# Kernel tuning notes

Measured on AMD Instinct MI355X. Metric: run time of the kernel, lower is better.

Reference implementation:

```python
import jax, jax.numpy as jnp
import numpy as np

N, D, H, L = 50000, 64, 4, 3
HD = D // H
E = 800000
EPS = 1e-5


def _layernorm(x, g, b):
    m = x.mean(-1, keepdims=True)
    v = ((x - m) ** 2).mean(-1, keepdims=True)
    return (x - m) * jax.lax.rsqrt(v + EPS) * g + b


def setup_inputs() -> dict:
    key = jax.random.key(0)
    ks = jax.random.split(key, 24)
    s = 0.05
    inp = {
        'feats': jax.random.normal(ks[0], (N, D), jnp.float32),
        'edge_index': jax.random.randint(ks[1], (2, E), 0, N, jnp.int64),
        'edge_attr': jax.random.uniform(ks[2], (E,), jnp.float32),
    }
    names = ['Wq', 'Wk', 'Wv', 'Wo', 'W1', 'W2']
    for i, n in enumerate(names):
        inp[n] = jax.random.normal(ks[3 + i], (L, D, D), jnp.float32) * s
    bnames = ['bq', 'bk', 'bv', 'bo', 'b1', 'b2']
    for i, n in enumerate(bnames):
        inp[n] = jnp.zeros((L, D), jnp.float32)
    inp['g1'] = jnp.ones((L, D), jnp.float32)
    inp['be1'] = jnp.zeros((L, D), jnp.float32)
    inp['g2'] = jnp.ones((L, D), jnp.float32)
    inp['be2'] = jnp.zeros((L, D), jnp.float32)
    return inp


def reference(feats, edge_index, edge_attr, Wq, bq, Wk, bk, Wv, bv, Wo, bo,
              W1, b1, W2, b2, g1, be1, g2, be2):
    row, col = edge_index[0], edge_index[1]  # source, destination nodes
    inv_sqrt = 1.0 / np.sqrt(HD).astype(np.float32)
    outs = []
    for l in range(L):
        # multi-head edge-indexed dot-product attention
        q = (feats @ Wq[l] + bq[l]).reshape(N, H, HD)
        k = (feats @ Wk[l] + bk[l]).reshape(N, H, HD)
        v = (feats @ Wv[l] + bv[l]).reshape(N, H, HD)
        scores = (q[col] * k[row]).sum(-1) * inv_sqrt       # [E, H]
        scores = scores * edge_attr[:, None]                # mult_attr modulation
        smax = jax.ops.segment_max(scores, col, num_segments=N)
        alpha = jnp.exp(scores - smax[col])
        denom = jax.ops.segment_sum(alpha, col, num_segments=N)
        alpha = alpha / denom[col]                          # scatter softmax
        agg = jax.ops.segment_sum(alpha[:, :, None] * v[row], col, num_segments=N)
        att = agg.reshape(N, D) @ Wo[l] + bo[l]
        feats = _layernorm(feats + att, g1[l], be1[l])      # res1 + norm1
        mlp = jax.nn.relu(feats @ W1[l] + b1[l]) @ W2[l] + b2[l]
        feats = _layernorm(feats + mlp, g2[l], be2[l])      # res2 + norm2
        outs.append(feats)
    return jnp.stack(outs)  # [L, N, D]
```

## Files before the change

kernel.cpp:

```cpp
#include <hip/hip_runtime.h>

#define NN 50000
#define DIM 64
#define NHEAD 4
#define NEDGE 800000
#define NLAYER 3
#define LN_EPS 1e-5f
#define SCAN_BLOCKS ((NN + 255) / 256)
#define ROWS 8

__device__ __forceinline__ float bcast(float x, int l) {
    return __uint_as_float(__builtin_amdgcn_readlane(__float_as_uint(x), l));
}

__device__ __forceinline__ unsigned int bf16rtn(float x) {
    unsigned int u = __float_as_uint(x);
    return (u + 0x7FFFu + ((u >> 16) & 1u)) >> 16;
}
__device__ __forceinline__ float blo(unsigned int u) {
    return __uint_as_float(u << 16);
}
__device__ __forceinline__ float bhi(unsigned int u) {
    return __uint_as_float(u & 0xFFFF0000u);
}


__global__ __launch_bounds__(256) void zero_kernel(int* __restrict__ p, int n) {
    int i = blockIdx.x * blockDim.x + threadIdx.x;
    if (i < n) p[i] = 0;
}

__global__ __launch_bounds__(256) void deg_kernel(const int* __restrict__ ei,
                                                  int* __restrict__ deg) {
    int e = blockIdx.x * blockDim.x + threadIdx.x;
    if (e < NEDGE) atomicAdd(&deg[ei[NEDGE + e]], 1);
}

__global__ __launch_bounds__(256) void scan1_kernel(const int* __restrict__ deg,
                                                    int* __restrict__ tmp,
                                                    int* __restrict__ bsum) {
    __shared__ int s[256];
    int t = threadIdx.x;
    int i = blockIdx.x * 256 + t;
    int v = (i < NN) ? deg[i] : 0;
    s[t] = v;
    __syncthreads();
    for (int off = 1; off < 256; off <<= 1) {
        int x = (t >= off) ? s[t - off] : 0;
        __syncthreads();
        s[t] += x;
        __syncthreads();
    }
    if (i < NN) tmp[i] = s[t] - v;
    if (t == 255) bsum[blockIdx.x] = s[255];
}

__global__ __launch_bounds__(256) void scan2_kernel(int* __restrict__ bsum) {
    __shared__ int s[256];
    int t = threadIdx.x;
    int v = (t < SCAN_BLOCKS) ? bsum[t] : 0;
    s[t] = v;
    __syncthreads();
    for (int off = 1; off < 256; off <<= 1) {
        int x = (t >= off) ? s[t - off] : 0;
        __syncthreads();
        s[t] += x;
        __syncthreads();
    }
    if (t < SCAN_BLOCKS) bsum[t] = s[t] - v;
}

__global__ __launch_bounds__(256) void scan3_kernel(const int* __restrict__ tmp,
                                                    const int* __restrict__ bsum,
                                                    int* __restrict__ rowptr,
                                                    int* __restrict__ cursor) {
    int i = blockIdx.x * 256 + threadIdx.x;
    if (i < NN) {
        int v = tmp[i] + bsum[i >> 8];
        rowptr[i] = v;
        cursor[i] = v;
    }
    if (i == 0) rowptr[NN] = NEDGE;
}

__global__ __launch_bounds__(256) void fill_kernel(const int* __restrict__ ei,
                                                   const float* __restrict__ attr,
                                                   int* __restrict__ cursor,
                                                   unsigned int* __restrict__ csr) {
    int e = blockIdx.x * blockDim.x + threadIdx.x;
    if (e >= NEDGE) return;
    int src = ei[e];
    int dst = ei[NEDGE + e];
    int idx = atomicAdd(&cursor[dst], 1);
    csr[idx] = (unsigned int)src | (bf16rtn(attr[e]) << 16);
}


__global__ __launch_bounds__(256) void qkv_kernel(
    const float* __restrict__ feats,
    const float* __restrict__ Wq, const float* __restrict__ Wk, const float* __restrict__ Wv,
    const float* __restrict__ bq, const float* __restrict__ bk, const float* __restrict__ bv,
    float* __restrict__ q, unsigned int* __restrict__ kvpk) {
    int wave = threadIdx.x >> 6;
    int lane = threadIdx.x & 63;
    int n0 = (blockIdx.x * 4 + wave) * ROWS;

    const float* rowp[ROWS];
    float qa[ROWS], ka[ROWS], va[ROWS];
    float biq = bq[lane], bik = bk[lane], biv = bv[lane];
    #pragma unroll
    for (int r = 0; r < ROWS; ++r) {
        int nu = __builtin_amdgcn_readfirstlane(min(n0 + r, NN - 1));
        rowp[r] = feats + (size_t)nu * DIM;
        qa[r] = biq; ka[r] = bik; va[r] = biv;
    }
    #pragma unroll
    for (int kk = 0; kk < DIM; ++kk) {
        float wq = Wq[kk * DIM + lane];
        float wk = Wk[kk * DIM + lane];
        float wv = Wv[kk * DIM + lane];
        #pragma unroll
        for (int r = 0; r < ROWS; ++r) {
            float x = rowp[r][kk];
            qa[r] = fmaf(x, wq, qa[r]);
            ka[r] = fmaf(x, wk, ka[r]);
            va[r] = fmaf(x, wv, va[r]);
        }
    }
    bool evenLane = (lane & 1) == 0;
    #pragma unroll
    for (int r = 0; r < ROWS; ++r) {
        int n = n0 + r;
        if (n < NN) q[n * DIM + lane] = qa[r] * 0.25f;
        unsigned int bk_ = bf16rtn(ka[r]);
        unsigned int bv_ = bf16rtn(va[r]);
        unsigned int nk = __shfl_xor(bk_, 1, 64);
        unsigned int nv = __shfl_xor(bv_, 1, 64);
        if (n < NN && evenLane) {
            kvpk[n * 64 + (lane >> 1)]      = bk_ | (nk << 16);
            kvpk[n * 64 + 32 + (lane >> 1)] = bv_ | (nv << 16);
        }
    }
}

__global__ __launch_bounds__(256) void attn_kernel(
    const int* __restrict__ rowptr, const unsigned int* __restrict__ csr,
    const float* __restrict__ q,
    const unsigned int* __restrict__ kvpk,
    float* __restrict__ agg) {
    int wave = threadIdx.x >> 6;
    int lane = threadIdx.x & 63;
    int quarter = lane >> 4;
    int slot = (lane >> 3) & 1;
    int g = lane & 7;
    int n = blockIdx.x * 16 + wave * 4 + quarter;
    if (n >= NN) return;

    float4 qa = *(const float4*)&q[n * DIM + 8 * g];
    float4 qb = *(const float4*)&q[n * DIM + 8 * g + 4];
    int beg = rowptr[n], end = rowptr[n + 1];

    float denom = 0.f;
    float a0 = 0.f, a1 = 0.f, a2 = 0.f, a3 = 0.f;
    float a4 = 0.f, a5 = 0.f, a6 = 0.f, a7 = 0.f;

    int ii = beg + slot;
    for (; ii + 2 < end; ii += 4) {
        unsigned int me0 = csr[ii];
        unsigned int me1 = csr[ii + 2];
        int src0 = (int)(me0 & 0xFFFFu);
        int src1 = (int)(me1 & 0xFFFFu);
        uint4 ku0 = *(const uint4*)&kvpk[src0 * 64 + 4 * g];
        uint4 vu0 = *(const uint4*)&kvpk[src0 * 64 + 32 + 4 * g];
        uint4 ku1 = *(const uint4*)&kvpk[src1 * 64 + 4 * g];
        uint4 vu1 = *(const uint4*)&kvpk[src1 * 64 + 32 + 4 * g];

        float p0 = qa.x * blo(ku0.x);
        p0 = fmaf(qa.y, bhi(ku0.x), p0);
        p0 = fmaf(qa.z, blo(ku0.y), p0);
        p0 = fmaf(qa.w, bhi(ku0.y), p0);
        p0 = fmaf(qb.x, blo(ku0.z), p0);
        p0 = fmaf(qb.y, bhi(ku0.z), p0);
        p0 = fmaf(qb.z, blo(ku0.w), p0);
        p0 = fmaf(qb.w, bhi(ku0.w), p0);
        float p1 = qa.x * blo(ku1.x);
        p1 = fmaf(qa.y, bhi(ku1.x), p1);
        p1 = fmaf(qa.z, blo(ku1.y), p1);
        p1 = fmaf(qa.w, bhi(ku1.y), p1);
        p1 = fmaf(qb.x, blo(ku1.z), p1);
        p1 = fmaf(qb.y, bhi(ku1.z), p1);
        p1 = fmaf(qb.z, blo(ku1.w), p1);
        p1 = fmaf(qb.w, bhi(ku1.w), p1);
        p0 += __shfl_xor(p0, 1, 64);
        p1 += __shfl_xor(p1, 1, 64);
        float w0 = __expf(p0 * bhi(me0));
        float w1 = __expf(p1 * bhi(me1));
        denom += w0 + w1;
        a0 = fmaf(w0, blo(vu0.x), a0); a0 = fmaf(w1, blo(vu1.x), a0);
        a1 = fmaf(w0, bhi(vu0.x), a1); a1 = fmaf(w1, bhi(vu1.x), a1);
        a2 = fmaf(w0, blo(vu0.y), a2); a2 = fmaf(w1, blo(vu1.y), a2);
        a3 = fmaf(w0, bhi(vu0.y), a3); a3 = fmaf(w1, bhi(vu1.y), a3);
        a4 = fmaf(w0, blo(vu0.z), a4); a4 = fmaf(w1, blo(vu1.z), a4);
        a5 = fmaf(w0, bhi(vu0.z), a5); a5 = fmaf(w1, bhi(vu1.z), a5);
        a6 = fmaf(w0, blo(vu0.w), a6); a6 = fmaf(w1, blo(vu1.w), a6);
        a7 = fmaf(w0, bhi(vu0.w), a7); a7 = fmaf(w1, bhi(vu1.w), a7);
    }
    for (; ii < end; ii += 2) {
        unsigned int me = csr[ii];
        int src = (int)(me & 0xFFFFu);
        float at = bhi(me);
        uint4 ku = *(const uint4*)&kvpk[src * 64 + 4 * g];
        uint4 vu = *(const uint4*)&kvpk[src * 64 + 32 + 4 * g];
        float p = qa.x * blo(ku.x);
        p = fmaf(qa.y, bhi(ku.x), p);
        p = fmaf(qa.z, blo(ku.y), p);
        p = fmaf(qa.w, bhi(ku.y), p);
        p = fmaf(qb.x, blo(ku.z), p);
        p = fmaf(qb.y, bhi(ku.z), p);
        p = fmaf(qb.z, blo(ku.w), p);
        p = fmaf(qb.w, bhi(ku.w), p);
        p += __shfl_xor(p, 1, 64);
        float w = __expf(p * at);
        denom += w;
        a0 = fmaf(w, blo(vu.x), a0);
        a1 = fmaf(w, bhi(vu.x), a1);
        a2 = fmaf(w, blo(vu.y), a2);
        a3 = fmaf(w, bhi(vu.y), a3);
        a4 = fmaf(w, blo(vu.z), a4);
        a5 = fmaf(w, bhi(vu.z), a5);
        a6 = fmaf(w, blo(vu.w), a6);
        a7 = fmaf(w, bhi(vu.w), a7);
    }
    denom += __shfl_xor(denom, 8, 64);
    a0 += __shfl_xor(a0, 8, 64);
    a1 += __shfl_xor(a1, 8, 64);
    a2 += __shfl_xor(a2, 8, 64);
    a3 += __shfl_xor(a3, 8, 64);
    a4 += __shfl_xor(a4, 8, 64);
    a5 += __shfl_xor(a5, 8, 64);
    a6 += __shfl_xor(a6, 8, 64);
    a7 += __shfl_xor(a7, 8, 64);

    if (slot == 0) {
        float inv = (denom > 0.f) ? 1.f / denom : 0.f;
        float4 o1; o1.x = a0 * inv; o1.y = a1 * inv; o1.z = a2 * inv; o1.w = a3 * inv;
        float4 o2; o2.x = a4 * inv; o2.y = a5 * inv; o2.z = a6 * inv; o2.w = a7 * inv;
        *(float4*)&agg[n * DIM + 8 * g] = o1;
        *(float4*)&agg[n * DIM + 8 * g + 4] = o2;
    }
}

__global__ __launch_bounds__(256) void post_kernel(
    const float* __restrict__ feats_in,
    const float* __restrict__ agg,
    const float* __restrict__ Wo, const float* __restrict__ bo,
    const float* __restrict__ W1, const float* __restrict__ b1,
    const float* __restrict__ W2, const float* __restrict__ b2,
    const float* __restrict__ g1, const float* __restrict__ be1,
    const float* __restrict__ g2, const float* __restrict__ be2,
    float* __restrict__ out) {
    int wave = threadIdx.x >> 6;
    int lane = threadIdx.x & 63;
    int n0 = (blockIdx.x * 4 + wave) * ROWS;

    float acc[ROWS], xin[ROWS];
    float bio = bo[lane];
    #pragma unroll
    for (int r = 0; r < ROWS; ++r) {
        int n = min(n0 + r, NN - 1);
        xin[r] = agg[n * DIM + lane];
        acc[r] = bio;
    }
    #pragma unroll
    for (int kk = 0; kk < DIM; ++kk) {
        float w = Wo[kk * DIM + lane];
        #pragma unroll
        for (int r = 0; r < ROWS; ++r)
            acc[r] = fmaf(bcast(xin[r], kk), w, acc[r]);
    }
    float gg1 = g1[lane], bb1 = be1[lane];
    #pragma unroll
    for (int r = 0; r < ROWS; ++r) {
        int n = min(n0 + r, NN - 1);
        float x = feats_in[n * DIM + lane] + acc[r];
        float s1 = x, s2 = x * x;
        #pragma unroll
        for (int o = 32; o >= 1; o >>= 1) {
            s1 += __shfl_xor(s1, o, 64);
            s2 += __shfl_xor(s2, o, 64);
        }
        float mean = s1 * (1.f / 64.f);
        float var = fmaf(-mean, mean, s2 * (1.f / 64.f));
        xin[r] = (x - mean) * rsqrtf(var + LN_EPS) * gg1 + bb1;
    }
    float bi1 = b1[lane];
    #pragma unroll
    for (int r = 0; r < ROWS; ++r) acc[r] = bi1;
    #pragma unroll
    for (int kk = 0; kk < DIM; ++kk) {
        float w = W1[kk * DIM + lane];
        #pragma unroll
        for (int r = 0; r < ROWS; ++r)
            acc[r] = fmaf(bcast(xin[r], kk), w, acc[r]);
    }
    float h[ROWS];
    #pragma unroll
    for (int r = 0; r < ROWS; ++r) h[r] = fmaxf(acc[r], 0.f);
    float bi2 = b2[lane];
    #pragma unroll
    for (int r = 0; r < ROWS; ++r) acc[r] = bi2;
    #pragma unroll
    for (int kk = 0; kk < DIM; ++kk) {
        float w = W2[kk * DIM + lane];
        #pragma unroll
        for (int r = 0; r < ROWS; ++r)
            acc[r] = fmaf(bcast(h[r], kk), w, acc[r]);
    }
    float gg2 = g2[lane], bb2 = be2[lane];
    #pragma unroll
    for (int r = 0; r < ROWS; ++r) {
        int n = n0 + r;
        float x2 = xin[r] + acc[r];
        float s1 = x2, s2 = x2 * x2;
        #pragma unroll
        for (int o = 32; o >= 1; o >>= 1) {
            s1 += __shfl_xor(s1, o, 64);
            s2 += __shfl_xor(s2, o, 64);
        }
        float mean = s1 * (1.f / 64.f);
        float var = fmaf(-mean, mean, s2 * (1.f / 64.f));
        if (n < NN)
            out[n * DIM + lane] = (x2 - mean) * rsqrtf(var + LN_EPS) * gg2 + bb2;
    }
}

extern "C" void kernel_launch(void* const* d_in, const int* in_sizes, int n_in,
                              void* d_out, int out_size, void* d_ws, size_t ws_size,
                              hipStream_t stream) {
    const float* feats = (const float*)d_in[0];
    const int*   ei    = (const int*)d_in[1];
    const float* attr  = (const float*)d_in[2];
    const float* Wq = (const float*)d_in[3];
    const float* Wk = (const float*)d_in[4];
    const float* Wv = (const float*)d_in[5];
    const float* Wo = (const float*)d_in[6];
    const float* W1 = (const float*)d_in[7];
    const float* W2 = (const float*)d_in[8];
    const float* bq = (const float*)d_in[9];
    const float* bk = (const float*)d_in[10];
    const float* bv = (const float*)d_in[11];
    const float* bo = (const float*)d_in[12];
    const float* b1 = (const float*)d_in[13];
    const float* b2 = (const float*)d_in[14];
    const float* g1  = (const float*)d_in[15];
    const float* be1 = (const float*)d_in[16];
    const float* g2  = (const float*)d_in[17];
    const float* be2 = (const float*)d_in[18];

    float* out = (float*)d_out;
    float* ws = (float*)d_ws;

    const size_t ND = (size_t)NN * DIM;
    float* q   = ws;
    float* agg = ws + ND;
    unsigned int* kvpk = (unsigned int*)(ws + 2 * ND);

    int* wi = (int*)(kvpk + (size_t)NN * 64);
    int* deg      = wi;
    int* cursor   = wi + NN;
    int* tmp      = wi + 2 * NN;
    int* bsum     = wi + 3 * NN;
    int* rowptr   = wi + 3 * NN + 256;
    unsigned int* csr = (unsigned int*)(rowptr + NN + 1);

    zero_kernel<<<(NN + 255) / 256, 256, 0, stream>>>(deg, NN);
    deg_kernel<<<(NEDGE + 255) / 256, 256, 0, stream>>>(ei, deg);
    scan1_kernel<<<SCAN_BLOCKS, 256, 0, stream>>>(deg, tmp, bsum);
    scan2_kernel<<<1, 256, 0, stream>>>(bsum);
    scan3_kernel<<<SCAN_BLOCKS, 256, 0, stream>>>(tmp, bsum, rowptr, cursor);
    fill_kernel<<<(NEDGE + 255) / 256, 256, 0, stream>>>(ei, attr, cursor, csr);

    const int rowBlocks = (NN + 4 * ROWS - 1) / (4 * ROWS);
    const int attnBlocks = (NN + 15) / 16;
    const float* fin = feats;
    for (int l = 0; l < NLAYER; ++l) {
        const size_t wOff = (size_t)l * DIM * DIM;
        const size_t bOff = (size_t)l * DIM;
        float* lout = out + (size_t)l * ND;

        qkv_kernel<<<rowBlocks, 256, 0, stream>>>(
            fin, Wq + wOff, Wk + wOff, Wv + wOff,
            bq + bOff, bk + bOff, bv + bOff, q, kvpk);

        attn_kernel<<<attnBlocks, 256, 0, stream>>>(rowptr, csr, q, kvpk, agg);

        post_kernel<<<rowBlocks, 256, 0, stream>>>(
            fin, agg,
            Wo + wOff, bo + bOff, W1 + wOff, b1 + bOff, W2 + wOff, b2 + bOff,
            g1 + bOff, be1 + bOff, g2 + bOff, be2 + bOff,
            lout);

        fin = lout;
    }
}
```

Measured before the change: 477.9 us.

## Split post kernel in two and read GEMM inputs via scalar loads

Splits the fused post-attention kernel into one kernel for the output projection plus first layernorm and another for the MLP plus second layernorm, with an intermediate buffer in the workspace. The row inputs to the first matmul of each kernel are now read through wave-uniform pointers (readfirstlane), so they can be fetched as scalar loads instead of a vector load followed by readlane broadcasts. This is meant to cut VALU and readlane overhead and register pressure in the inner FMA loops. The cost is an extra kernel launch and a full N×D intermediate written and read back through global memory.

```diff
diff --git a/kernel.cpp b/kernel.cpp
--- a/kernel.cpp
+++ b/kernel.cpp
@@ -250,25 +250,23 @@
     }
 }
 
-__global__ __launch_bounds__(256) void post_kernel(
+__global__ __launch_bounds__(256) void post1_kernel(
     const float* __restrict__ feats_in,
     const float* __restrict__ agg,
     const float* __restrict__ Wo, const float* __restrict__ bo,
-    const float* __restrict__ W1, const float* __restrict__ b1,
-    const float* __restrict__ W2, const float* __restrict__ b2,
     const float* __restrict__ g1, const float* __restrict__ be1,
-    const float* __restrict__ g2, const float* __restrict__ be2,
-    float* __restrict__ out) {
+    float* __restrict__ fm) {
     int wave = threadIdx.x >> 6;
     int lane = threadIdx.x & 63;
     int n0 = (blockIdx.x * 4 + wave) * ROWS;
 
-    float acc[ROWS], xin[ROWS];
+    const float* rowp[ROWS];
+    float acc[ROWS];
     float bio = bo[lane];
     #pragma unroll
     for (int r = 0; r < ROWS; ++r) {
-        int n = min(n0 + r, NN - 1);
-        xin[r] = agg[n * DIM + lane];
+        int nu = __builtin_amdgcn_readfirstlane(min(n0 + r, NN - 1));
+        rowp[r] = agg + (size_t)nu * DIM;
         acc[r] = bio;
     }
     #pragma unroll
@@ -276,7 +274,7 @@
         float w = Wo[kk * DIM + lane];
         #pragma unroll
         for (int r = 0; r < ROWS; ++r)
-            acc[r] = fmaf(bcast(xin[r], kk), w, acc[r]);
+            acc[r] = fmaf(rowp[r][kk], w, acc[r]);
     }
     float gg1 = g1[lane], bb1 = be1[lane];
     #pragma unroll
@@ -291,17 +289,37 @@
         }
         float mean = s1 * (1.f / 64.f);
         float var = fmaf(-mean, mean, s2 * (1.f / 64.f));
-        xin[r] = (x - mean) * rsqrtf(var + LN_EPS) * gg1 + bb1;
-    }
+        if (n0 + r < NN)
+            fm[(size_t)(n0 + r) * DIM + lane] =
+                (x - mean) * rsqrtf(var + LN_EPS) * gg1 + bb1;
+    }
+}
+
+__global__ __launch_bounds__(256) void post2_kernel(
+    const float* __restrict__ fm,
+    const float* __restrict__ W1, const float* __restrict__ b1,
+    const float* __restrict__ W2, const float* __restrict__ b2,
+    const float* __restrict__ g2, const float* __restrict__ be2,
+    float* __restrict__ out) {
+    int wave = threadIdx.x >> 6;
+    int lane = threadIdx.x & 63;
+    int n0 = (blockIdx.x * 4 + wave) * ROWS;
+
+    const float* rowp[ROWS];
+    float acc[ROWS];
     float bi1 = b1[lane];
     #pragma unroll
-    for (int r = 0; r < ROWS; ++r) acc[r] = bi1;
+    for (int r = 0; r < ROWS; ++r) {
+        int nu = __builtin_amdgcn_readfirstlane(min(n0 + r, NN - 1));
+        rowp[r] = fm + (size_t)nu * DIM;
+        acc[r] = bi1;
+    }
     #pragma unroll
     for (int kk = 0; kk < DIM; ++kk) {
         float w = W1[kk * DIM + lane];
         #pragma unroll
         for (int r = 0; r < ROWS; ++r)
-            acc[r] = fmaf(bcast(xin[r], kk), w, acc[r]);
+            acc[r] = fmaf(rowp[r][kk], w, acc[r]);
     }
     float h[ROWS];
     #pragma unroll
@@ -319,8 +337,8 @@
     float gg2 = g2[lane], bb2 = be2[lane];
     #pragma unroll
     for (int r = 0; r < ROWS; ++r) {
-        int n = n0 + r;
-        float x2 = xin[r] + acc[r];
+        int n = min(n0 + r, NN - 1);
+        float x2 = fm[(size_t)n * DIM + lane] + acc[r];
         float s1 = x2, s2 = x2 * x2;
         #pragma unroll
         for (int o = 32; o >= 1; o >>= 1) {
@@ -329,8 +347,9 @@
         }
         float mean = s1 * (1.f / 64.f);
         float var = fmaf(-mean, mean, s2 * (1.f / 64.f));
-        if (n < NN)
-            out[n * DIM + lane] = (x2 - mean) * rsqrtf(var + LN_EPS) * gg2 + bb2;
+        if (n0 + r < NN)
+            out[(size_t)(n0 + r) * DIM + lane] =
+                (x2 - mean) * rsqrtf(var + LN_EPS) * gg2 + bb2;
     }
 }
 
@@ -363,7 +382,8 @@
     const size_t ND = (size_t)NN * DIM;
     float* q   = ws;
     float* agg = ws + ND;
-    unsigned int* kvpk = (unsigned int*)(ws + 2 * ND);
+    float* fmb = ws + 2 * ND;
+    unsigned int* kvpk = (unsigned int*)(ws + 3 * ND);
 
     int* wi = (int*)(kvpk + (size_t)NN * 64);
     int* deg      = wi;
@@ -394,11 +414,12 @@
 
         attn_kernel<<<attnBlocks, 256, 0, stream>>>(rowptr, csr, q, kvpk, agg);
 
-        post_kernel<<<rowBlocks, 256, 0, stream>>>(
-            fin, agg,
-            Wo + wOff, bo + bOff, W1 + wOff, b1 + bOff, W2 + wOff, b2 + bOff,
-            g1 + bOff, be1 + bOff, g2 + bOff, be2 + bOff,
-            lout);
+        post1_kernel<<<rowBlocks, 256, 0, stream>>>(
+            fin, agg, Wo + wOff, bo + bOff, g1 + bOff, be1 + bOff, fmb);
+
+        post2_kernel<<<rowBlocks, 256, 0, stream>>>(
+            fmb, W1 + wOff, b1 + bOff, W2 + wOff, b2 + bOff,
+            g2 + bOff, be2 + bOff, lout);
 
         fin = lout;
     }
```

New measurement: 468.0 us. 2.1% less time.
